# Performance work log

Measured on AMD Instinct MI355X. Metric: run time of the kernel, lower is better.

The kernel has to match this reference:

```python
import jax, jax.numpy as jnp
import numpy as np

SCALE = 1.0

def setup_inputs() -> dict:
    key = jax.random.key(0)
    k1, k2 = jax.random.split(key)
    N, C = 262144, 1000
    outputs = jax.random.normal(k1, (N, C), dtype=jnp.float32)
    targets = jax.random.randint(k2, (N,), 0, C, dtype=jnp.int64)
    cost_matrix = jnp.zeros((C, C), dtype=jnp.float32)
    return {"outputs": outputs, "cost_matrix": cost_matrix, "targets": targets}

def reference(outputs, cost_matrix, targets):
    # log-softmax over classes, single stable pass
    log_probs = jax.nn.log_softmax(outputs, axis=1)          # [N, C]
    predicted = jnp.argmax(log_probs, axis=1)                # [N]
    # vectorized replacement of the per-sample Python loop: scatter-add counts
    cm = cost_matrix.at[targets, predicted].add(1.0)         # [C, C]
    C = cm.shape[0]
    cm = cm * (1.0 - jnp.eye(C, dtype=cm.dtype))             # zero diagonal
    cm = cm / jnp.max(cm) * SCALE + 1.0
    n = jnp.arange(targets.shape[0])
    gather_log_probs = log_probs[n, targets]                 # [N]
    gather_costs = cm[targets, predicted]                    # [N]
    loss = -jnp.mean(gather_log_probs * gather_costs)
    return loss
```

## Files before the change

kernel.cpp:

```cpp
#include <hip/hip_runtime.h>
#include <math.h>

#define NROWS 262144
#define NC    1000
#define SCALEF 1.0f

#define WS_GLP_OFF   4000000
#define WS_PAIR_OFF  (4000000 + NROWS * 4)
#define WS_SCAL_OFF  (4000000 + NROWS * 8)

__global__ __launch_bounds__(256) void k_init(const float* __restrict__ cost_in,
                                              float* __restrict__ cm,
                                              double* __restrict__ losssum,
                                              unsigned* __restrict__ maxbits) {
    int i = blockIdx.x * 256 + threadIdx.x;
    if (i < NC * NC) cm[i] = cost_in[i];
    if (i == 0) { *losssum = 0.0; *maxbits = 0u; }
}

__global__ __launch_bounds__(256) void k_row(const float* __restrict__ outs,
                                             const int* __restrict__ targets,
                                             float* __restrict__ cm,
                                             float* __restrict__ glp,
                                             int* __restrict__ pair) {
    int row  = blockIdx.x * 4 + (threadIdx.x >> 6);
    int lane = threadIdx.x & 63;
    if (row >= NROWS) return;

    const float* rp = outs + (size_t)row * NC;
    int t = targets[row];
    float tval = rp[t];

    float4 f0 = *(const float4*)(rp + 4 * lane);
    float4 f1 = *(const float4*)(rp + 256 + 4 * lane);
    float4 f2 = *(const float4*)(rp + 512 + 4 * lane);
    float4 f3;
    bool has3 = (4 * lane) < (NC - 768);
    if (has3) f3 = *(const float4*)(rp + 768 + 4 * lane);
    else      f3 = make_float4(-INFINITY, -INFINITY, -INFINITY, -INFINITY);

    float v[16] = {f0.x, f0.y, f0.z, f0.w,
                   f1.x, f1.y, f1.z, f1.w,
                   f2.x, f2.y, f2.z, f2.w,
                   f3.x, f3.y, f3.z, f3.w};

    float mx = -INFINITY;
    int   ami = 0x7fffffff;
    #pragma unroll
    for (int q = 0; q < 16; ++q) {
        int idx = 256 * (q >> 2) + 4 * lane + (q & 3);
        float val = v[q];
        if (val > mx || (val == mx && idx < ami)) { mx = val; ami = idx; }
    }
    #pragma unroll
    for (int off = 32; off; off >>= 1) {
        float omx = __shfl_xor(mx, off, 64);
        int   oi  = __shfl_xor(ami, off, 64);
        if (omx > mx || (omx == mx && oi < ami)) { mx = omx; ami = oi; }
    }

    float s = 0.f;
    #pragma unroll
    for (int q = 0; q < 16; ++q) s += __expf(v[q] - mx);
    #pragma unroll
    for (int off = 32; off; off >>= 1) s += __shfl_xor(s, off, 64);

    if (lane == 0) {
        float lp_t = tval - mx - __logf(s);
        glp[row]  = lp_t;
        pair[row] = t * NC + ami;
        atomicAdd(&cm[t * NC + ami], 1.0f);
    }
}

__global__ __launch_bounds__(256) void k_cmmax(const float* __restrict__ cm,
                                               unsigned* __restrict__ maxbits) {
    int idx = blockIdx.x * 256 + threadIdx.x;
    float val = 0.f;
    if (idx < NC * NC) {
        int r = idx / NC;
        int c = idx - r * NC;
        val = (r == c) ? 0.f : cm[idx];
    }
    #pragma unroll
    for (int off = 32; off; off >>= 1) val = fmaxf(val, __shfl_xor(val, off, 64));
    if ((threadIdx.x & 63) == 0)
        atomicMax(maxbits, __float_as_uint(val));
}

__global__ __launch_bounds__(256) void k_loss(const float* __restrict__ cm,
                                              const float* __restrict__ glp,
                                              const int* __restrict__ pair,
                                              const unsigned* __restrict__ maxbits,
                                              double* __restrict__ losssum) {
    int n = blockIdx.x * 256 + threadIdx.x;
    double part = 0.0;
    if (n < NROWS) {
        int pr = pair[n];
        int t = pr / NC;
        int p = pr - t * NC;
        float cost;
        if (t == p) cost = 1.0f;
        else        cost = cm[pr] / __uint_as_float(*maxbits) * SCALEF + 1.0f;
        part = (double)glp[n] * (double)cost;
    }
    #pragma unroll
    for (int off = 32; off; off >>= 1) part += __shfl_xor(part, off, 64);
    if ((threadIdx.x & 63) == 0) atomicAdd(losssum, part);
}

__global__ void k_final(const double* __restrict__ losssum, float* __restrict__ out) {
    out[0] = (float)(-(*losssum) / (double)NROWS);
}

extern "C" void kernel_launch(void* const* d_in, const int* in_sizes, int n_in,
                              void* d_out, int out_size, void* d_ws, size_t ws_size,
                              hipStream_t stream) {
    const float* outs    = (const float*)d_in[0];
    const float* cost_in = (const float*)d_in[1];
    const int*   targets = (const int*)d_in[2];

    char* ws = (char*)d_ws;
    float*    cm      = (float*)ws;
    float*    glp     = (float*)(ws + WS_GLP_OFF);
    int*      pair    = (int*)(ws + WS_PAIR_OFF);
    double*   losssum = (double*)(ws + WS_SCAL_OFF);
    unsigned* maxbits = (unsigned*)(ws + WS_SCAL_OFF + 8);

    k_init<<<(NC * NC + 255) / 256, 256, 0, stream>>>(cost_in, cm, losssum, maxbits);
    k_row<<<NROWS / 4, 256, 0, stream>>>(outs, targets, cm, glp, pair);
    k_cmmax<<<(NC * NC + 255) / 256, 256, 0, stream>>>(cm, maxbits);
    k_loss<<<(NROWS + 255) / 256, 256, 0, stream>>>(cm, glp, pair, maxbits, losssum);
    k_final<<<1, 1, 0, stream>>>(losssum, (float*)d_out);
}
```

Before: 1.527 ms.

## Accumulate per-cell log-prob sums to compute loss over confusion cells

```diff
diff --git a/kernel.cpp b/kernel.cpp
--- a/kernel.cpp
+++ b/kernel.cpp
@@ -3,33 +3,31 @@
 
 #define NROWS 262144
 #define NC    1000
+#define NCELL (NC * NC)
 #define SCALEF 1.0f
 
-#define WS_GLP_OFF   4000000
-#define WS_PAIR_OFF  (4000000 + NROWS * 4)
-#define WS_SCAL_OFF  (4000000 + NROWS * 8)
+#define WS_S_OFF    4000000
+#define WS_SCAL_OFF 8000000
 
 __global__ __launch_bounds__(256) void k_init(const float* __restrict__ cost_in,
                                               float* __restrict__ cm,
+                                              float* __restrict__ S,
                                               double* __restrict__ losssum,
-                                              unsigned* __restrict__ maxbits) {
+                                              unsigned* __restrict__ scal) {
     int i = blockIdx.x * 256 + threadIdx.x;
-    if (i < NC * NC) cm[i] = cost_in[i];
-    if (i == 0) { *losssum = 0.0; *maxbits = 0u; }
+    if (i < NCELL) { cm[i] = cost_in[i]; S[i] = 0.f; }
+    if (i == 0) { *losssum = 0.0; scal[0] = 0u; scal[1] = 0u; }
 }
 
 __global__ __launch_bounds__(256) void k_row(const float* __restrict__ outs,
                                              const int* __restrict__ targets,
                                              float* __restrict__ cm,
-                                             float* __restrict__ glp,
-                                             int* __restrict__ pair) {
+                                             float* __restrict__ S) {
     int row  = blockIdx.x * 4 + (threadIdx.x >> 6);
     int lane = threadIdx.x & 63;
-    if (row >= NROWS) return;
 
     const float* rp = outs + (size_t)row * NC;
     int t = targets[row];
-    float tval = rp[t];
 
     float4 f0 = *(const float4*)(rp + 4 * lane);
     float4 f1 = *(const float4*)(rp + 256 + 4 * lane);
@@ -38,6 +36,8 @@
     bool has3 = (4 * lane) < (NC - 768);
     if (has3) f3 = *(const float4*)(rp + 768 + 4 * lane);
     else      f3 = make_float4(-INFINITY, -INFINITY, -INFINITY, -INFINITY);
+
+    float tval = rp[t];
 
     float v[16] = {f0.x, f0.y, f0.z, f0.w,
                    f1.x, f1.y, f1.z, f1.w,
@@ -67,50 +67,62 @@
 
     if (lane == 0) {
         float lp_t = tval - mx - __logf(s);
-        glp[row]  = lp_t;
-        pair[row] = t * NC + ami;
-        atomicAdd(&cm[t * NC + ami], 1.0f);
+        int cell = t * NC + ami;
+        atomicAdd(&cm[cell], 1.0f);
+        atomicAdd(&S[cell], lp_t);
     }
 }
 
 __global__ __launch_bounds__(256) void k_cmmax(const float* __restrict__ cm,
                                                unsigned* __restrict__ maxbits) {
-    int idx = blockIdx.x * 256 + threadIdx.x;
+    __shared__ float red[4];
     float val = 0.f;
-    if (idx < NC * NC) {
+    for (int idx = blockIdx.x * 256 + threadIdx.x; idx < NCELL; idx += gridDim.x * 256) {
         int r = idx / NC;
         int c = idx - r * NC;
-        val = (r == c) ? 0.f : cm[idx];
+        float x = (r == c) ? 0.f : cm[idx];
+        val = fmaxf(val, x);
     }
     #pragma unroll
     for (int off = 32; off; off >>= 1) val = fmaxf(val, __shfl_xor(val, off, 64));
-    if ((threadIdx.x & 63) == 0)
+    if ((threadIdx.x & 63) == 0) red[threadIdx.x >> 6] = val;
+    __syncthreads();
+    if (threadIdx.x == 0) {
+        val = fmaxf(fmaxf(red[0], red[1]), fmaxf(red[2], red[3]));
         atomicMax(maxbits, __float_as_uint(val));
+    }
 }
 
 __global__ __launch_bounds__(256) void k_loss(const float* __restrict__ cm,
-                                              const float* __restrict__ glp,
-                                              const int* __restrict__ pair,
+                                              const float* __restrict__ S,
                                               const unsigned* __restrict__ maxbits,
-                                              double* __restrict__ losssum) {
-    int n = blockIdx.x * 256 + threadIdx.x;
+                                              double* __restrict__ losssum,
+                                              unsigned* __restrict__ counter,
+                                              float* __restrict__ out) {
+    __shared__ double red[4];
+    float inv_mx = SCALEF / __uint_as_float(*maxbits);
     double part = 0.0;
-    if (n < NROWS) {
-        int pr = pair[n];
-        int t = pr / NC;
-        int p = pr - t * NC;
-        float cost;
-        if (t == p) cost = 1.0f;
-        else        cost = cm[pr] / __uint_as_float(*maxbits) * SCALEF + 1.0f;
-        part = (double)glp[n] * (double)cost;
+    for (int idx = blockIdx.x * 256 + threadIdx.x; idx < NCELL; idx += gridDim.x * 256) {
+        int r = idx / NC;
+        int c = idx - r * NC;
+        float sv = S[idx];
+        float cost = (r == c) ? 1.0f : fmaf(cm[idx], inv_mx, 1.0f);
+        part += (double)(sv * cost);
     }
     #pragma unroll
     for (int off = 32; off; off >>= 1) part += __shfl_xor(part, off, 64);
-    if ((threadIdx.x & 63) == 0) atomicAdd(losssum, part);
-}
-
-__global__ void k_final(const double* __restrict__ losssum, float* __restrict__ out) {
-    out[0] = (float)(-(*losssum) / (double)NROWS);
+    if ((threadIdx.x & 63) == 0) red[threadIdx.x >> 6] = part;
+    __syncthreads();
+    if (threadIdx.x == 0) {
+        part = red[0] + red[1] + red[2] + red[3];
+        atomicAdd(losssum, part);
+        __threadfence();
+        unsigned prev = atomicAdd(counter, 1u);
+        if (prev == gridDim.x - 1) {
+            double total = atomicAdd(losssum, 0.0);
+            out[0] = (float)(-total / (double)NROWS);
+        }
+    }
 }
 
 extern "C" void kernel_launch(void* const* d_in, const int* in_sizes, int n_in,
@@ -122,14 +134,13 @@
 
     char* ws = (char*)d_ws;
     float*    cm      = (float*)ws;
-    float*    glp     = (float*)(ws + WS_GLP_OFF);
-    int*      pair    = (int*)(ws + WS_PAIR_OFF);
+    float*    S       = (float*)(ws + WS_S_OFF);
     double*   losssum = (double*)(ws + WS_SCAL_OFF);
     unsigned* maxbits = (unsigned*)(ws + WS_SCAL_OFF + 8);
+    unsigned* counter = (unsigned*)(ws + WS_SCAL_OFF + 12);
 
-    k_init<<<(NC * NC + 255) / 256, 256, 0, stream>>>(cost_in, cm, losssum, maxbits);
-    k_row<<<NROWS / 4, 256, 0, stream>>>(outs, targets, cm, glp, pair);
-    k_cmmax<<<(NC * NC + 255) / 256, 256, 0, stream>>>(cm, maxbits);
-    k_loss<<<(NROWS + 255) / 256, 256, 0, stream>>>(cm, glp, pair, maxbits, losssum);
-    k_final<<<1, 1, 0, stream>>>(losssum, (float*)d_out);
+    k_init<<<(NCELL + 255) / 256, 256, 0, stream>>>(cost_in, cm, S, losssum, maxbits);
+    k_row<<<NROWS / 4, 256, 0, stream>>>(outs, targets, cm, S);
+    k_cmmax<<<512, 256, 0, stream>>>(cm, maxbits);
+    k_loss<<<512, 256, 0, stream>>>(cm, S, maxbits, losssum, counter, (float*)d_out);
 }
```

New measurement: 1.339 ms. -12.3%, faster.
